# Kernel optimization log

Measured on AMD Instinct MI355X. Metric: run time of the kernel, lower is better.

Reference implementation:

```python
import jax, jax.numpy as jnp
import numpy as np
import itertools

F = 20        # field_size
D = 16        # embedding_size / output_dims
H = 2         # num_hash
NB = 500000   # num_buckets
B = 4096      # batch
NI = F * (F - 1) // 2  # 190 pairwise interactions


def _interact_indexes(field_size):
    # For each field i, indices of the C(F,2) combinations that contain i -> [F, F-1]
    combos = list(itertools.combinations(range(field_size), 2))
    idx = [[j for j, c in enumerate(combos) if i in c] for i in range(field_size)]
    return np.asarray(idx, dtype=np.int32)


def setup_inputs() -> dict:
    key = jax.random.key(0)
    k0, k1, k2, k3, k4, k5 = jax.random.split(key, 6)
    return {
        "origin_embeddings": jax.random.normal(k0, (B, F, D), jnp.float32),
        "codebook": jax.random.normal(k1, (NB, D), jnp.float32) * 0.01,
        "W_transform": jax.random.normal(k2, (H * D, D), jnp.float32) * 0.05,
        "senet_w1": jax.random.normal(k3, (F * D, F * D), jnp.float32) * 0.02,
        "senet_w2": jax.random.normal(k4, (F * D, NI), jnp.float32) * 0.02,
        # Precomputed hash bucket ids (stands in for the StrongHash of string tokens)
        "hash_idx": jax.random.randint(k5, (H, B, NI), 0, NB, dtype=jnp.int32),
        "interact_indexes": jnp.asarray(_interact_indexes(F)),
    }


def reference(origin_embeddings, codebook, W_transform, senet_w1, senet_w2, hash_idx, interact_indexes):
    b = origin_embeddings.shape[0]
    # multi-hash codebook gathers (hash-share: one codebook): [H, B, NI, D]
    gathered = codebook[hash_idx]
    # merge_mode='concat' over hash functions -> [B, NI, H*D]
    emb = jnp.concatenate([gathered[i] for i in range(gathered.shape[0])], axis=-1)
    # hash_merge_final_transform: Dense(output_dims, no bias) -> [B, NI, D]
    emb = jnp.einsum('bne,ed->bnd', emb, W_transform)
    # SENET (bit squeeze, ratio 1.0, vector excitation, no activation) over origin embeddings
    z = origin_embeddings.reshape(b, -1)          # [B, F*D]
    w = (z @ senet_w1) @ senet_w2                 # [B, NI]
    # gather each field's interactions and weighted-sum ('senetsum')
    field_emb = emb[:, interact_indexes]          # [B, F, F-1, D]
    field_w = w[:, interact_indexes][..., None]   # [B, F, F-1, 1]
    out = jnp.sum(field_emb * field_w, axis=-2)   # [B, F, D]
    return out
```

## Files before the change

### kernel.cpp

```cpp
#include <hip/hip_runtime.h>

#define FF 20
#define NI 190
#define NIP 192
#define BB 4096
#define FD 320
#define RSTR 36

__global__ __launch_bounds__(192) void k_w12(const float* __restrict__ w1,
                                             const float* __restrict__ w2,
                                             float* __restrict__ W12p) {
    __shared__ float srow[FD];
    int r = blockIdx.x;
    for (int j = threadIdx.x; j < FD; j += 192) srow[j] = w1[r * FD + j];
    __syncthreads();
    int c = threadIdx.x;
    float acc = 0.f;
    if (c < NI) {
        for (int k = 0; k < FD; ++k) acc += srow[k] * w2[k * NI + c];
    }
    W12p[r * NIP + c] = acc;
}

__global__ __launch_bounds__(256) void k_w(const float* __restrict__ z,
                                           const float* __restrict__ W12p,
                                           float* __restrict__ wout) {
    __shared__ float zT[32][68];
    __shared__ float Ws[32][64];
    int b0 = blockIdx.x * 64;
    int c0 = blockIdx.y * 64;
    int t = threadIdx.x;
    int tr = t >> 4, tc = t & 15;
    float acc[4][4];
#pragma unroll
    for (int i = 0; i < 4; ++i)
#pragma unroll
        for (int j = 0; j < 4; ++j) acc[i][j] = 0.f;

    for (int k0 = 0; k0 < FD; k0 += 32) {
#pragma unroll
        for (int s = 0; s < 2; ++s) {
            int task = t + s * 256;
            int row = task >> 3, ch = task & 7;
            float4 v = *(const float4*)&z[(b0 + row) * FD + k0 + ch * 4];
            zT[ch * 4 + 0][row] = v.x;
            zT[ch * 4 + 1][row] = v.y;
            zT[ch * 4 + 2][row] = v.z;
            zT[ch * 4 + 3][row] = v.w;
        }
#pragma unroll
        for (int s = 0; s < 2; ++s) {
            int task = t + s * 256;
            int kr = task >> 4, cq = task & 15;
            *(float4*)&Ws[kr][cq * 4] = *(const float4*)&W12p[(k0 + kr) * NIP + c0 + cq * 4];
        }
        __syncthreads();
#pragma unroll
        for (int k = 0; k < 32; ++k) {
            float4 zb = *(const float4*)&zT[k][tr * 4];
            float4 wv = *(const float4*)&Ws[k][tc * 4];
            float zz[4] = {zb.x, zb.y, zb.z, zb.w};
            float ww[4] = {wv.x, wv.y, wv.z, wv.w};
#pragma unroll
            for (int i = 0; i < 4; ++i)
#pragma unroll
                for (int j = 0; j < 4; ++j) acc[i][j] += zz[i] * ww[j];
        }
        __syncthreads();
    }
#pragma unroll
    for (int i = 0; i < 4; ++i) {
        float4 v = make_float4(acc[i][0], acc[i][1], acc[i][2], acc[i][3]);
        *(float4*)&wout[(b0 + tr * 4 + i) * NIP + c0 + tc * 4] = v;
    }
}

__global__ __launch_bounds__(256) void k_main(const float* __restrict__ cb,
                                              const float* __restrict__ Wt,
                                              const int* __restrict__ hidx,
                                              const int* __restrict__ iidx,
                                              const float* __restrict__ wbuf,
                                              float* __restrict__ out) {
    __shared__ float s_rows[NI * RSTR];
    __shared__ float s_w[NI];
    __shared__ int s_pii[FF * (FF - 1)];

    int t = threadIdx.x;
    int b = blockIdx.x;

    for (int j = t; j < NI; j += 256) s_w[j] = wbuf[b * NIP + j];
    for (int j = t; j < FF * (FF - 1); j += 256) s_pii[j] = iidx[j];

    int d = t & 15;
    float Wr[32];
#pragma unroll
    for (int k = 0; k < 32; ++k) Wr[k] = Wt[k * 16 + d];

    const float4* cb4 = (const float4*)cb;
#pragma unroll
    for (int it = 0; it < 6; ++it) {
        int tt = t + it * 256;
        if (tt < NI * 8) {
            int pair = tt >> 3;
            int half = (tt >> 2) & 1;
            int chunk = tt & 3;
            int row = hidx[(half * BB + b) * NI + pair];
            float4 v = cb4[row * 4 + chunk];
            *(float4*)&s_rows[pair * RSTR + half * 16 + chunk * 4] = v;
        }
    }
    __syncthreads();

    int pp = t >> 4;
#pragma unroll
    for (int rnd = 0; rnd < 12; ++rnd) {
        int pair = rnd * 16 + pp;
        if (pair < NI) {
            const float4* r4 = (const float4*)&s_rows[pair * RSTR];
            float acc = 0.f;
#pragma unroll
            for (int c = 0; c < 8; ++c) {
                float4 v = r4[c];
                acc += v.x * Wr[c * 4 + 0];
                acc += v.y * Wr[c * 4 + 1];
                acc += v.z * Wr[c * 4 + 2];
                acc += v.w * Wr[c * 4 + 3];
            }
            s_rows[pair * RSTR + d] = acc * s_w[pair];
        }
    }
    __syncthreads();

    for (int o = t; o < FD; o += 256) {
        int i = o >> 4;
        int dd = o & 15;
        float acc = 0.f;
#pragma unroll
        for (int s = 0; s < FF - 1; ++s) {
            int j = s_pii[i * (FF - 1) + s];
            acc += s_rows[j * RSTR + dd];
        }
        out[b * FD + o] = acc;
    }
}

extern "C" void kernel_launch(void* const* d_in, const int* in_sizes, int n_in,
                              void* d_out, int out_size, void* d_ws, size_t ws_size,
                              hipStream_t stream) {
    const float* origin = (const float*)d_in[0];
    const float* cb     = (const float*)d_in[1];
    const float* Wt     = (const float*)d_in[2];
    const float* w1     = (const float*)d_in[3];
    const float* w2     = (const float*)d_in[4];
    const int*   hidx   = (const int*)d_in[5];
    const int*   iidx   = (const int*)d_in[6];
    float* out = (float*)d_out;

    float* W12p = (float*)d_ws;
    float* wbuf = W12p + FD * NIP;

    k_w12<<<FD, 192, 0, stream>>>(w1, w2, W12p);
    dim3 gw(BB / 64, 3);
    k_w<<<gw, 256, 0, stream>>>(origin, W12p, wbuf);
    k_main<<<BB, 256, 0, stream>>>(cb, Wt, hidx, iidx, wbuf, out);
}
```

Measured before the change: 152.2 us.

## Reorder weighted field sums before the hash-merge transform in the main kernel

The main kernel no longer applies the 32x16 transform to each of the 190 pairs. Instead, for each field, each thread group sums the 19 weighted codebook rows per hash, then applies the transform once per field (20 per sample). The block grows to 320 threads, one per output element, and the transform weights are staged in shared memory. This cuts per-pair matrix work and the staging of all gathered rows in shared memory. In exchange, every codebook row is gathered twice, once for each field that uses it, with scalar loads instead of float4 loads, which raises gather traffic.

```diff
diff --git a/kernel.cpp b/kernel.cpp
--- a/kernel.cpp
+++ b/kernel.cpp
@@ -5,7 +5,6 @@
 #define NIP 192
 #define BB 4096
 #define FD 320
-#define RSTR 36
 
 __global__ __launch_bounds__(192) void k_w12(const float* __restrict__ w1,
                                              const float* __restrict__ w2,
@@ -75,73 +74,52 @@
     }
 }
 
-__global__ __launch_bounds__(256) void k_main(const float* __restrict__ cb,
+#define SA(f, h, d) ((f) * 33 + (h) * 16 + (d))
+__global__ __launch_bounds__(320) void k_main(const float* __restrict__ cb,
                                               const float* __restrict__ Wt,
                                               const int* __restrict__ hidx,
                                               const int* __restrict__ iidx,
                                               const float* __restrict__ wbuf,
                                               float* __restrict__ out) {
-    __shared__ float s_rows[NI * RSTR];
+    __shared__ int s_i0[NI], s_i1[NI];
     __shared__ float s_w[NI];
-    __shared__ int s_pii[FF * (FF - 1)];
+    __shared__ int s_plist[FF * 19];
+    __shared__ float s_W[32 * 16];
+    __shared__ float s_acc[19 * 33 + 2 * 16 + 16];
 
     int t = threadIdx.x;
     int b = blockIdx.x;
 
-    for (int j = t; j < NI; j += 256) s_w[j] = wbuf[b * NIP + j];
-    for (int j = t; j < FF * (FF - 1); j += 256) s_pii[j] = iidx[j];
-
-    int d = t & 15;
-    float Wr[32];
-#pragma unroll
-    for (int k = 0; k < 32; ++k) Wr[k] = Wt[k * 16 + d];
-
-    const float4* cb4 = (const float4*)cb;
-#pragma unroll
-    for (int it = 0; it < 6; ++it) {
-        int tt = t + it * 256;
-        if (tt < NI * 8) {
-            int pair = tt >> 3;
-            int half = (tt >> 2) & 1;
-            int chunk = tt & 3;
-            int row = hidx[(half * BB + b) * NI + pair];
-            float4 v = cb4[row * 4 + chunk];
-            *(float4*)&s_rows[pair * RSTR + half * 16 + chunk * 4] = v;
-        }
+    if (t < NI) {
+        s_i0[t] = hidx[b * NI + t];
+        s_i1[t] = hidx[(BB + b) * NI + t];
+        s_w[t] = wbuf[b * NIP + t];
     }
+    for (int j = t; j < FF * 19; j += 320) s_plist[j] = iidx[j];
+    for (int j = t; j < 512; j += 320) s_W[j] = Wt[j];
     __syncthreads();
 
-    int pp = t >> 4;
+    int f = t >> 4, d = t & 15;
+    const int* pl = &s_plist[f * 19];
+    float a0 = 0.f, a1 = 0.f;
 #pragma unroll
-    for (int rnd = 0; rnd < 12; ++rnd) {
-        int pair = rnd * 16 + pp;
-        if (pair < NI) {
-            const float4* r4 = (const float4*)&s_rows[pair * RSTR];
-            float acc = 0.f;
-#pragma unroll
-            for (int c = 0; c < 8; ++c) {
-                float4 v = r4[c];
-                acc += v.x * Wr[c * 4 + 0];
-                acc += v.y * Wr[c * 4 + 1];
-                acc += v.z * Wr[c * 4 + 2];
-                acc += v.w * Wr[c * 4 + 3];
-            }
-            s_rows[pair * RSTR + d] = acc * s_w[pair];
-        }
+    for (int j = 0; j < 19; ++j) {
+        int p = pl[j];
+        float wv = s_w[p];
+        a0 += wv * cb[s_i0[p] * 16 + d];
+        a1 += wv * cb[s_i1[p] * 16 + d];
     }
+    s_acc[SA(f, 0, d)] = a0;
+    s_acc[SA(f, 1, d)] = a1;
     __syncthreads();
 
-    for (int o = t; o < FD; o += 256) {
-        int i = o >> 4;
-        int dd = o & 15;
-        float acc = 0.f;
+    float r = 0.f;
 #pragma unroll
-        for (int s = 0; s < FF - 1; ++s) {
-            int j = s_pii[i * (FF - 1) + s];
-            acc += s_rows[j * RSTR + dd];
-        }
-        out[b * FD + o] = acc;
+    for (int k = 0; k < 16; ++k) {
+        r += s_acc[SA(f, 0, k)] * s_W[k * 16 + d];
+        r += s_acc[SA(f, 1, k)] * s_W[(16 + k) * 16 + d];
     }
+    out[b * FD + t] = r;
 }
 
 extern "C" void kernel_launch(void* const* d_in, const int* in_sizes, int n_in,
@@ -162,5 +140,5 @@
     k_w12<<<FD, 192, 0, stream>>>(w1, w2, W12p);
     dim3 gw(BB / 64, 3);
     k_w<<<gw, 256, 0, stream>>>(origin, W12p, wbuf);
-    k_main<<<BB, 256, 0, stream>>>(cb, Wt, hidx, iidx, wbuf, out);
+    k_main<<<BB, 320, 0, stream>>>(cb, Wt, hidx, iidx, wbuf, out);
 }
```

Result: faster. 144.8 us (-4.9%).
